# Optimization experiments

Measured on AMD Instinct MI355X. Metric: run time of the kernel, lower is better.

The kernel has to match this reference:

```python
import jax, jax.numpy as jnp
import numpy as np
from jax import lax

WINDOW_SIZE = 11
SIGMA = 1.5


def gaussian_window(channel, size=WINDOW_SIZE, sigma=SIGMA):
    coords = jnp.arange(size, dtype=jnp.float32) - size // 2
    g = jnp.exp(-coords ** 2 / (2.0 * sigma ** 2))
    g = g / g.sum()
    w2d = g[:, None] * g[None, :]                       # [size, size]
    return jnp.broadcast_to(w2d, (channel, 1, size, size))  # OIHW, depthwise


def depthwise_conv(x, w, c):
    pad = WINDOW_SIZE // 2
    return lax.conv_general_dilated(
        x, w,
        window_strides=(1, 1),
        padding=[(pad, pad), (pad, pad)],
        dimension_numbers=('NCHW', 'OIHW', 'NCHW'),
        feature_group_count=c,
    )


def setup_inputs() -> dict:
    key = jax.random.key(0)
    k1, k2 = jax.random.split(key)
    pred = jax.random.uniform(k1, (32, 3, 512, 512), dtype=jnp.float32)
    target = jax.random.uniform(k2, (32, 3, 512, 512), dtype=jnp.float32)
    return {"pred": pred, "target": target}


def reference(pred, target):
    c = pred.shape[1]
    w = gaussian_window(c).astype(pred.dtype)
    mu1 = depthwise_conv(pred, w, c)
    mu2 = depthwise_conv(target, w, c)
    mu1_sq = mu1 * mu1
    mu2_sq = mu2 * mu2
    mu1_mu2 = mu1 * mu2
    sigma1_sq = depthwise_conv(pred * pred, w, c) - mu1_sq
    sigma2_sq = depthwise_conv(target * target, w, c) - mu2_sq
    sigma12 = depthwise_conv(pred * target, w, c) - mu1_mu2
    C1 = 0.01 ** 2
    C2 = 0.03 ** 2
    ssim_map = (2.0 * mu1_mu2 + C1) * (2.0 * sigma12 + C2) / (
        (mu1_sq + mu2_sq + C1) * (sigma1_sq + sigma2_sq + C2) + 1e-08)
    return 1.0 - ssim_map.mean()
```

## Files before the change

### kernel.cpp

```cpp
#include <hip/hip_runtime.h>

typedef float f32x2 __attribute__((ext_vector_type(2)));

#define IMG_W 512
#define IMG_H 512
#define TY 8
#define PLANES 96
#define NPIX (32ll * 3 * 512 * 512)
#define NACC 64

#define WG_INIT { 0.00102838f, 0.00759876f, 0.03600077f, 0.10936069f, \
                  0.21300553f, 0.26601172f, 0.21300553f, 0.10936069f, \
                  0.03600077f, 0.00759876f, 0.00102838f }

#define SLAB_ATOMS 272
#define SLAB_BYTES (SLAB_ATOMS * 16)

__device__ __forceinline__ int pmap(int at) {
    const int par = at & 1;
    return (at & ~15) | (par << 3) | (((at >> 1) & 7) ^ (par << 2));
}

__global__ __launch_bounds__(512)
void ssim_main(const float* __restrict__ pred, const float* __restrict__ targ,
               double* __restrict__ acc) {
    const float WG[11] = WG_INIT;

    __shared__ __align__(16) unsigned char ldsraw[8 * SLAB_BYTES];
    __shared__ float wsum[8];

    const int tid   = threadIdx.x;
    const int x     = tid;
    const int plane = blockIdx.y;
    const int y0    = blockIdx.x * TY;
    const size_t base = (size_t)plane * (IMG_W * IMG_H);
    const float* pCol = pred + base + x;
    const float* tCol = targ + base + x;

    if (tid < 64) {
        const int s   = tid >> 3;
        const int idx = tid & 7;
        const int at  = (idx < 4) ? idx : (256 + idx);
        *(float4*)(ldsraw + s * SLAB_BYTES + pmap(at) * 16) =
            (float4){0.f, 0.f, 0.f, 0.f};
    }

    float pv[TY + 10], tv[TY + 10];
#pragma unroll
    for (int iy = 0; iy < TY + 10; ++iy) {
        const int y = y0 - 5 + iy;
        pv[iy] = 0.f; tv[iy] = 0.f;
        if ((unsigned)y < (unsigned)IMG_H) {
            pv[iy] = pCol[(size_t)y * IMG_W];
            tv[iy] = tCol[(size_t)y * IMG_W];
        }
    }

    f32x2 A[4][4];
#pragma unroll
    for (int m = 0; m < 4; ++m)
#pragma unroll
        for (int rp = 0; rp < 4; ++rp) A[m][rp] = (f32x2){0.f, 0.f};

#pragma unroll
    for (int iy = 0; iy < TY + 10; ++iy) {
        const float p = pv[iy], t = tv[iy];
        const float ss = __builtin_fmaf(t, t, p * p);
        const float pt = p * t;
        const f32x2 vs[4] = { {p,p}, {t,t}, {ss,ss}, {pt,pt} };
#pragma unroll
        for (int rp = 0; rp < 4; ++rp) {
            const int a = iy - 2 * rp;
            if (a < 0 || a > 11) continue;
            const float w0 = (a <= 10) ? WG[a] : 0.f;
            const float w1 = (a >= 1)  ? WG[a - 1] : 0.f;
            const f32x2 w = (f32x2){w0, w1};
#pragma unroll
            for (int m = 0; m < 4; ++m)
                A[m][rp] = __builtin_elementwise_fma(vs[m], w, A[m][rp]);
        }
    }

    const int g   = tid & 127;
    const int rpl = tid >> 7;
    const int wat = (x + 8) >> 1;
    const int wof = pmap(wat) * 16 + ((x + 8) & 1) * 8;
    int rof[8];
#pragma unroll
    for (int q = 0; q < 8; ++q) rof[q] = pmap(2 * g + 1 + q) * 16;

    f32x2 H[4][4];
#pragma unroll
    for (int phase = 0; phase < 2; ++phase) {
        if (phase) __syncthreads();
#pragma unroll
        for (int ml = 0; ml < 2; ++ml)
#pragma unroll
            for (int rp = 0; rp < 4; ++rp)
                *(f32x2*)(ldsraw + (ml * 4 + rp) * SLAB_BYTES + wof) =
                    A[phase * 2 + ml][rp];
        __syncthreads();

#pragma unroll
        for (int ml = 0; ml < 2; ++ml) {
            const unsigned char* slab = ldsraw + (ml * 4 + rpl) * SLAB_BYTES;
            f32x2 win[16];
#pragma unroll
            for (int q = 0; q < 8; ++q) {
                const float4 v = *(const float4*)(slab + rof[q]);
                win[2 * q]     = (f32x2){v.x, v.y};
                win[2 * q + 1] = (f32x2){v.z, v.w};
            }
            f32x2 hacc[4];
#pragma unroll
            for (int c = 0; c < 4; ++c) hacc[c] = (f32x2){0.f, 0.f};
#pragma unroll
            for (int k = 0; k < 11; ++k) {
                const f32x2 wk2 = (f32x2){WG[k], WG[k]};
#pragma unroll
                for (int c = 0; c < 4; ++c) {
                    asm("v_pk_fma_f32 %0, %1, %2, %0"
                        : "+v"(hacc[c])
                        : "v"(win[c + 1 + k]), "v"(wk2));
                }
            }
#pragma unroll
            for (int c = 0; c < 4; ++c) H[phase * 2 + ml][c] = hacc[c];
        }
    }

    const float C1 = 1e-4f, C2 = 9e-4f;
    float lsum = 0.f;
#pragma unroll
    for (int c = 0; c < 4; ++c) {
        const f32x2 mu1 = H[0][c], mu2 = H[1][c];
        const f32x2 S   = H[2][c], P  = H[3][c];
        const f32x2 mu12 = mu1 * mu2;
        const f32x2 musq = mu1 * mu1 + mu2 * mu2;
        const f32x2 num = (mu12 + mu12 + (f32x2){C1, C1}) *
                          ((P - mu12) + (P - mu12) + (f32x2){C2, C2});
        const f32x2 den = (musq + (f32x2){C1, C1}) *
                          (S - musq + (f32x2){C2, C2}) + (f32x2){1e-8f, 1e-8f};
        lsum += num.x * __builtin_amdgcn_rcpf(den.x);
        lsum += num.y * __builtin_amdgcn_rcpf(den.y);
    }

#pragma unroll
    for (int off = 32; off > 0; off >>= 1)
        lsum += __shfl_down(lsum, off);
    if ((tid & 63) == 0) wsum[tid >> 6] = lsum;
    __syncthreads();
    if (tid == 0) {
        float s = 0.f;
#pragma unroll
        for (int i = 0; i < 8; ++i) s += wsum[i];
        atomicAdd(&acc[blockIdx.x & (NACC - 1)], (double)s);
    }
}

__global__ void ssim_final(const double* __restrict__ acc, float* __restrict__ out) {
    const int i = threadIdx.x;
    double s = acc[i];
#pragma unroll
    for (int off = 32; off > 0; off >>= 1)
        s += __shfl_down(s, off);
    if (i == 0) out[0] = 1.0f - (float)(s * (1.0 / (double)NPIX));
}

extern "C" void kernel_launch(void* const* d_in, const int* in_sizes, int n_in,
                              void* d_out, int out_size, void* d_ws, size_t ws_size,
                              hipStream_t stream) {
    const float* pred = (const float*)d_in[0];
    const float* targ = (const float*)d_in[1];
    double* acc = (double*)d_ws;

    hipMemsetAsync(acc, 0, NACC * sizeof(double), stream);

    dim3 grid(IMG_H / TY, PLANES);
    ssim_main<<<grid, 512, 0, stream>>>(pred, targ, acc);
    ssim_final<<<1, 64, 0, stream>>>(acc, (float*)d_out);
}
```

Measured before the change: 231.3 us.

## Process eight row strips per block with sliding halo reuse and fused final reduction

Each block now loops over eight consecutive 8-row strips of a plane instead of one. It keeps the 10-row vertical halo in registers and loads only 8 new rows per strip, prefetching them before the horizontal pass. The separate final-reduction kernel is replaced by a last-block-done counter inside the main kernel, which removes one launch. The grid shrinks from 6144 to 768 blocks, which cuts redundant halo loads and per-block setup but reduces the parallelism available to hide latency. The inline-asm packed FMA is also replaced with the builtin elementwise FMA.

```diff
diff --git a/kernel.cpp b/kernel.cpp
--- a/kernel.cpp
+++ b/kernel.cpp
@@ -5,9 +5,11 @@
 #define IMG_W 512
 #define IMG_H 512
 #define TY 8
+#define SPB 8
 #define PLANES 96
 #define NPIX (32ll * 3 * 512 * 512)
 #define NACC 64
+#define NBLOCKS (8 * PLANES)
 
 #define WG_INIT { 0.00102838f, 0.00759876f, 0.03600077f, 0.10936069f, \
                   0.21300553f, 0.26601172f, 0.21300553f, 0.10936069f, \
@@ -23,16 +25,18 @@
 
 __global__ __launch_bounds__(512)
 void ssim_main(const float* __restrict__ pred, const float* __restrict__ targ,
-               double* __restrict__ acc) {
+               double* __restrict__ acc, float* __restrict__ out) {
     const float WG[11] = WG_INIT;
 
     __shared__ __align__(16) unsigned char ldsraw[8 * SLAB_BYTES];
-    __shared__ float wsum[8];
+    __shared__ double wsum[8];
+    __shared__ int islast;
 
     const int tid   = threadIdx.x;
     const int x     = tid;
     const int plane = blockIdx.y;
-    const int y0    = blockIdx.x * TY;
+    const int grp   = blockIdx.x;
+    const int yb    = grp * (TY * SPB);
     const size_t base = (size_t)plane * (IMG_W * IMG_H);
     const float* pCol = pred + base + x;
     const float* tCol = targ + base + x;
@@ -48,36 +52,11 @@
     float pv[TY + 10], tv[TY + 10];
 #pragma unroll
     for (int iy = 0; iy < TY + 10; ++iy) {
-        const int y = y0 - 5 + iy;
+        const int y = yb - 5 + iy;
         pv[iy] = 0.f; tv[iy] = 0.f;
         if ((unsigned)y < (unsigned)IMG_H) {
             pv[iy] = pCol[(size_t)y * IMG_W];
             tv[iy] = tCol[(size_t)y * IMG_W];
-        }
-    }
-
-    f32x2 A[4][4];
-#pragma unroll
-    for (int m = 0; m < 4; ++m)
-#pragma unroll
-        for (int rp = 0; rp < 4; ++rp) A[m][rp] = (f32x2){0.f, 0.f};
-
-#pragma unroll
-    for (int iy = 0; iy < TY + 10; ++iy) {
-        const float p = pv[iy], t = tv[iy];
-        const float ss = __builtin_fmaf(t, t, p * p);
-        const float pt = p * t;
-        const f32x2 vs[4] = { {p,p}, {t,t}, {ss,ss}, {pt,pt} };
-#pragma unroll
-        for (int rp = 0; rp < 4; ++rp) {
-            const int a = iy - 2 * rp;
-            if (a < 0 || a > 11) continue;
-            const float w0 = (a <= 10) ? WG[a] : 0.f;
-            const float w1 = (a >= 1)  ? WG[a - 1] : 0.f;
-            const f32x2 w = (f32x2){w0, w1};
-#pragma unroll
-            for (int m = 0; m < 4; ++m)
-                A[m][rp] = __builtin_elementwise_fma(vs[m], w, A[m][rp]);
         }
     }
 
@@ -89,82 +68,134 @@
 #pragma unroll
     for (int q = 0; q < 8; ++q) rof[q] = pmap(2 * g + 1 + q) * 16;
 
-    f32x2 H[4][4];
-#pragma unroll
-    for (int phase = 0; phase < 2; ++phase) {
-        if (phase) __syncthreads();
-#pragma unroll
-        for (int ml = 0; ml < 2; ++ml)
-#pragma unroll
-            for (int rp = 0; rp < 4; ++rp)
-                *(f32x2*)(ldsraw + (ml * 4 + rp) * SLAB_BYTES + wof) =
-                    A[phase * 2 + ml][rp];
-        __syncthreads();
-
-#pragma unroll
-        for (int ml = 0; ml < 2; ++ml) {
-            const unsigned char* slab = ldsraw + (ml * 4 + rpl) * SLAB_BYTES;
-            f32x2 win[16];
-#pragma unroll
-            for (int q = 0; q < 8; ++q) {
-                const float4 v = *(const float4*)(slab + rof[q]);
-                win[2 * q]     = (f32x2){v.x, v.y};
-                win[2 * q + 1] = (f32x2){v.z, v.w};
+    double dsum = 0.0;
+
+#pragma unroll 1
+    for (int s = 0; s < SPB; ++s) {
+        f32x2 A[4][4];
+#pragma unroll
+        for (int m = 0; m < 4; ++m)
+#pragma unroll
+            for (int rp = 0; rp < 4; ++rp) A[m][rp] = (f32x2){0.f, 0.f};
+
+#pragma unroll
+        for (int iy = 0; iy < TY + 10; ++iy) {
+            const float p = pv[iy], t = tv[iy];
+            const float ss = __builtin_fmaf(t, t, p * p);
+            const float pt = p * t;
+            const f32x2 vs[4] = { {p,p}, {t,t}, {ss,ss}, {pt,pt} };
+#pragma unroll
+            for (int rp = 0; rp < 4; ++rp) {
+                const int a = iy - 2 * rp;
+                if (a < 0 || a > 11) continue;
+                const float w0 = (a <= 10) ? WG[a] : 0.f;
+                const float w1 = (a >= 1)  ? WG[a - 1] : 0.f;
+                const f32x2 w = (f32x2){w0, w1};
+#pragma unroll
+                for (int m = 0; m < 4; ++m)
+                    A[m][rp] = __builtin_elementwise_fma(vs[m], w, A[m][rp]);
             }
-            f32x2 hacc[4];
-#pragma unroll
-            for (int c = 0; c < 4; ++c) hacc[c] = (f32x2){0.f, 0.f};
-#pragma unroll
-            for (int k = 0; k < 11; ++k) {
-                const f32x2 wk2 = (f32x2){WG[k], WG[k]};
-#pragma unroll
-                for (int c = 0; c < 4; ++c) {
-                    asm("v_pk_fma_f32 %0, %1, %2, %0"
-                        : "+v"(hacc[c])
-                        : "v"(win[c + 1 + k]), "v"(wk2));
+        }
+
+        if (s + 1 < SPB) {
+#pragma unroll
+            for (int i = 0; i < 10; ++i) { pv[i] = pv[i + 8]; tv[i] = tv[i + 8]; }
+            const int yn = yb + (s + 1) * TY;
+#pragma unroll
+            for (int iy = 10; iy < TY + 10; ++iy) {
+                const int y = yn - 5 + iy;
+                pv[iy] = 0.f; tv[iy] = 0.f;
+                if ((unsigned)y < (unsigned)IMG_H) {
+                    pv[iy] = pCol[(size_t)y * IMG_W];
+                    tv[iy] = tCol[(size_t)y * IMG_W];
                 }
             }
-#pragma unroll
-            for (int c = 0; c < 4; ++c) H[phase * 2 + ml][c] = hacc[c];
-        }
-    }
-
-    const float C1 = 1e-4f, C2 = 9e-4f;
-    float lsum = 0.f;
-#pragma unroll
-    for (int c = 0; c < 4; ++c) {
-        const f32x2 mu1 = H[0][c], mu2 = H[1][c];
-        const f32x2 S   = H[2][c], P  = H[3][c];
-        const f32x2 mu12 = mu1 * mu2;
-        const f32x2 musq = mu1 * mu1 + mu2 * mu2;
-        const f32x2 num = (mu12 + mu12 + (f32x2){C1, C1}) *
-                          ((P - mu12) + (P - mu12) + (f32x2){C2, C2});
-        const f32x2 den = (musq + (f32x2){C1, C1}) *
-                          (S - musq + (f32x2){C2, C2}) + (f32x2){1e-8f, 1e-8f};
-        lsum += num.x * __builtin_amdgcn_rcpf(den.x);
-        lsum += num.y * __builtin_amdgcn_rcpf(den.y);
+        }
+
+        f32x2 H[4][4];
+#pragma unroll
+        for (int phase = 0; phase < 2; ++phase) {
+            if (phase | s) __syncthreads();
+#pragma unroll
+            for (int ml = 0; ml < 2; ++ml)
+#pragma unroll
+                for (int rp = 0; rp < 4; ++rp)
+                    *(f32x2*)(ldsraw + (ml * 4 + rp) * SLAB_BYTES + wof) =
+                        A[phase * 2 + ml][rp];
+            __syncthreads();
+
+#pragma unroll
+            for (int ml = 0; ml < 2; ++ml) {
+                const unsigned char* slab =
+                    ldsraw + (ml * 4 + rpl) * SLAB_BYTES;
+                f32x2 win[16];
+#pragma unroll
+                for (int q = 0; q < 8; ++q) {
+                    const float4 v = *(const float4*)(slab + rof[q]);
+                    win[2 * q]     = (f32x2){v.x, v.y};
+                    win[2 * q + 1] = (f32x2){v.z, v.w};
+                }
+                f32x2 hacc[4];
+#pragma unroll
+                for (int c = 0; c < 4; ++c) hacc[c] = (f32x2){0.f, 0.f};
+#pragma unroll
+                for (int k = 0; k < 11; ++k) {
+                    const f32x2 wk = (f32x2){WG[k], WG[k]};
+#pragma unroll
+                    for (int c = 0; c < 4; ++c)
+                        hacc[c] = __builtin_elementwise_fma(win[c + 1 + k],
+                                                            wk, hacc[c]);
+                }
+#pragma unroll
+                for (int c = 0; c < 4; ++c) H[phase * 2 + ml][c] = hacc[c];
+            }
+        }
+
+        const float C1 = 1e-4f, C2 = 9e-4f;
+        float lsum = 0.f;
+#pragma unroll
+        for (int c = 0; c < 4; ++c) {
+            const f32x2 mu1 = H[0][c], mu2 = H[1][c];
+            const f32x2 S   = H[2][c], P  = H[3][c];
+            const f32x2 mu12 = mu1 * mu2;
+            const f32x2 musq = mu1 * mu1 + mu2 * mu2;
+            const f32x2 num = (mu12 + mu12 + (f32x2){C1, C1}) *
+                              ((P - mu12) + (P - mu12) + (f32x2){C2, C2});
+            const f32x2 den = (musq + (f32x2){C1, C1}) *
+                              (S - musq + (f32x2){C2, C2}) +
+                              (f32x2){1e-8f, 1e-8f};
+            lsum += num.x * __builtin_amdgcn_rcpf(den.x);
+            lsum += num.y * __builtin_amdgcn_rcpf(den.y);
+        }
+        dsum += (double)lsum;
     }
 
 #pragma unroll
     for (int off = 32; off > 0; off >>= 1)
-        lsum += __shfl_down(lsum, off);
-    if ((tid & 63) == 0) wsum[tid >> 6] = lsum;
+        dsum += __shfl_down(dsum, off);
+    if ((tid & 63) == 0) wsum[tid >> 6] = dsum;
     __syncthreads();
+    unsigned int* cnt = (unsigned int*)(acc + NACC);
     if (tid == 0) {
-        float s = 0.f;
-#pragma unroll
-        for (int i = 0; i < 8; ++i) s += wsum[i];
-        atomicAdd(&acc[blockIdx.x & (NACC - 1)], (double)s);
-    }
-}
-
-__global__ void ssim_final(const double* __restrict__ acc, float* __restrict__ out) {
-    const int i = threadIdx.x;
-    double s = acc[i];
-#pragma unroll
-    for (int off = 32; off > 0; off >>= 1)
-        s += __shfl_down(s, off);
-    if (i == 0) out[0] = 1.0f - (float)(s * (1.0 / (double)NPIX));
+        double bs = 0.0;
+#pragma unroll
+        for (int i = 0; i < 8; ++i) bs += wsum[i];
+        atomicAdd(&acc[(plane * 8 + grp) & (NACC - 1)], bs);
+        __threadfence();
+        const unsigned int old = atomicAdd(cnt, 1u);
+        islast = (old == NBLOCKS - 1);
+    }
+    __syncthreads();
+
+    if (islast && tid < 64) {
+        __threadfence();
+        double v = atomicAdd(&acc[tid], 0.0);
+#pragma unroll
+        for (int off = 32; off > 0; off >>= 1)
+            v += __shfl_down(v, off);
+        if (tid == 0)
+            out[0] = 1.0f - (float)(v * (1.0 / (double)NPIX));
+    }
 }
 
 extern "C" void kernel_launch(void* const* d_in, const int* in_sizes, int n_in,
@@ -174,9 +205,8 @@
     const float* targ = (const float*)d_in[1];
     double* acc = (double*)d_ws;
 
-    hipMemsetAsync(acc, 0, NACC * sizeof(double), stream);
-
-    dim3 grid(IMG_H / TY, PLANES);
-    ssim_main<<<grid, 512, 0, stream>>>(pred, targ, acc);
-    ssim_final<<<1, 64, 0, stream>>>(acc, (float*)d_out);
+    hipMemsetAsync(acc, 0, (NACC + 1) * sizeof(double), stream);
+
+    dim3 grid(8, PLANES);
+    ssim_main<<<grid, 512, 0, stream>>>(pred, targ, acc, (float*)d_out);
 }
```

Result: slower. 269.4 us (+16.5%).
